# Optimization experiments

Measured on AMD Instinct MI355X. Metric: run time of the kernel, lower is better.

Reference implementation:

```python
import jax, jax.numpy as jnp
import numpy as np

B, T, C, H = 128, 256, 1024, 64


def setup_inputs() -> dict:
    key = jax.random.key(0)
    k1, k2, k3, k4 = jax.random.split(key, 4)
    # Glorot-ish scale for weights
    s = 1.0 / np.sqrt(C)
    return {
        "x": jax.random.normal(k1, (B, T, C), dtype=jnp.float32),
        "Wk": jax.random.normal(k2, (C, H), dtype=jnp.float32) * s,
        "Wq": jax.random.normal(k3, (C, H), dtype=jnp.float32) * s,
        "Wv": jax.random.normal(k4, (C, H), dtype=jnp.float32) * s,
    }


def reference(x, Wk, Wq, Wv):
    # Projections (no bias, matching use_bias=False)
    k = jnp.einsum("btc,ch->bth", x, Wk)  # [B,T,H]
    q = jnp.einsum("btc,ch->bth", x, Wq)
    v = jnp.einsum("btc,ch->bth", x, Wv)
    scale = k.shape[-1] ** -0.5
    wei = jnp.einsum("bth,bsh->bts", q, k) * scale  # [B,T,T]
    t = x.shape[1]
    causal = jnp.tril(jnp.ones((t, t), dtype=bool))
    wei = jnp.where(causal, wei, -jnp.inf)
    wei = jax.nn.softmax(wei, axis=-1)
    # dropout is identity at inference
    out = jnp.einsum("bts,bsh->bth", wei, v)  # [B,T,H]
    return out
```

## Files before the change

kernel.cpp:

```cpp
#include <hip/hip_runtime.h>
#include <hip/hip_bf16.h>

typedef __bf16 v8bf __attribute__((ext_vector_type(8)));
typedef float f32x16 __attribute__((ext_vector_type(16)));
typedef unsigned int uint;
typedef unsigned short ushort;

#define GLOAD16(gsrc, ldst)                                                       \
  __builtin_amdgcn_global_load_lds(                                               \
      (const __attribute__((address_space(1))) unsigned int*)(gsrc),              \
      (__attribute__((address_space(3))) unsigned int*)(ldst), 16, 0, 0)

__device__ inline f32x16 zero16() {
  f32x16 z;
#pragma unroll
  for (int i = 0; i < 16; i++) z[i] = 0.f;
  return z;
}

__device__ inline uint pack_bf16(float a, float b) {
  union { __bf16 h[2]; uint u; } c;
  c.h[0] = (__bf16)a;
  c.h[1] = (__bf16)b;
  return c.u;
}

__global__ void prep_wt(const float* __restrict__ Wq, const float* __restrict__ Wk,
                        const float* __restrict__ Wv, char* __restrict__ Wt_s) {
  __shared__ __bf16 tile[64][74];
  const int mat = blockIdx.x >> 4;
  const int c0 = (blockIdx.x & 15) * 64;
  const float* src = (mat == 0) ? Wq : (mat == 1) ? Wk : Wv;
  const int t = threadIdx.x;
  {
    const int r = t >> 2;
    const int ch = (t & 3) * 16;
    const float4* s4 = (const float4*)(src + (size_t)(c0 + r) * 64 + ch);
#pragma unroll
    for (int j = 0; j < 4; j++) {
      float4 f = s4[j];
      tile[r][ch + 4 * j + 0] = (__bf16)f.x;
      tile[r][ch + 4 * j + 1] = (__bf16)f.y;
      tile[r][ch + 4 * j + 2] = (__bf16)f.z;
      tile[r][ch + 4 * j + 3] = (__bf16)f.w;
    }
  }
  __syncthreads();
  const int h = t >> 2;
  const int cc = (t & 3) * 16;
  union { __bf16 o[16]; uint4 u[2]; } pk;
#pragma unroll
  for (int j = 0; j < 16; j++) pk.o[j] = tile[cc + j][h];
  const int n = mat * 64 + h;
  char* base = Wt_s + (size_t)n * 2048 + (c0 >> 6) * 128;
  const int bc = cc * 2;
  *(uint4*)(base + ((bc) ^ ((n & 7) << 4))) = pk.u[0];
  *(uint4*)(base + ((bc + 16) ^ ((n & 7) << 4))) = pk.u[1];
}

__launch_bounds__(256, 2)
__global__ void proj_kernel(const float* __restrict__ x, const char* __restrict__ Wt_s,
                            __bf16* __restrict__ KQV) {
  __shared__ char lds[65536];
  char* A0 = lds;
  char* A1 = lds + 8192;
  char* W0 = lds + 16384;
  char* W1 = lds + 40960;

  const int tid = threadIdx.x;
  const int lane = tid & 63;
  const int wave = tid >> 6;
  const int wm = wave >> 1;
  const int wn = wave & 1;
  const int row0 = blockIdx.x * 64;

  const int sr = tid >> 2;
  const int sc = tid & 3;
  const float4* xp = (const float4*)(x + (size_t)(row0 + sr) * 1024 + sc * 16);

  f32x16 acc[3];
#pragma unroll
  for (int i = 0; i < 3; i++) acc[i] = zero16();

  float4 rA[4], rB[4];

#define LOADA(rr, t)                                                              \
  {                                                                               \
    _Pragma("unroll") for (int j = 0; j < 4; j++) rr[j] = xp[(t) * 16 + j];       \
  }

#define GW(t, Wbuf)                                                               \
  {                                                                               \
    _Pragma("unroll") for (int j = 0; j < 6; j++) {                               \
      int idx = wave * 64 + j * 256 + lane;                                       \
      GLOAD16(Wt_s + (size_t)(idx >> 3) * 2048 + (t) * 128 + (idx & 7) * 16,      \
              Wbuf + wave * 1024 + j * 4096);                                     \
    }                                                                             \
  }

#define CVTWRITE(rr, Abuf)                                                        \
  {                                                                               \
    union { __bf16 h[16]; uint4 u[2]; } cv;                                       \
    _Pragma("unroll") for (int j = 0; j < 4; j++) {                               \
      cv.h[4 * j + 0] = (__bf16)rr[j].x;                                          \
      cv.h[4 * j + 1] = (__bf16)rr[j].y;                                          \
      cv.h[4 * j + 2] = (__bf16)rr[j].z;                                          \
      cv.h[4 * j + 3] = (__bf16)rr[j].w;                                          \
    }                                                                             \
    *(uint4*)(Abuf + sr * 128 + ((sc * 32) ^ ((sr & 7) << 4))) = cv.u[0];         \
    *(uint4*)(Abuf + sr * 128 + ((sc * 32 + 16) ^ ((sr & 7) << 4))) = cv.u[1];    \
  }

#define MMA(Abuf, Wbuf)                                                           \
  {                                                                               \
    _Pragma("unroll") for (int ks = 0; ks < 4; ks++) {                            \
      int arow = wm * 32 + (lane & 31);                                           \
      int kb = ks * 32 + ((lane >> 5) << 4);                                      \
      v8bf av = *(const v8bf*)(Abuf + arow * 128 + (kb ^ ((arow & 7) << 4)));     \
      _Pragma("unroll") for (int nf = 0; nf < 3; nf++) {                          \
        int brow = wn * 96 + nf * 32 + (lane & 31);                               \
        v8bf bv = *(const v8bf*)(Wbuf + brow * 128 + (kb ^ ((brow & 7) << 4)));   \
        acc[nf] = __builtin_amdgcn_mfma_f32_32x32x16_bf16(av, bv, acc[nf], 0, 0, 0); \
      }                                                                           \
    }                                                                             \
  }

  GW(0, W0);
  LOADA(rA, 0);
  CVTWRITE(rA, A0);
  __syncthreads();

  for (int t = 0; t < 16; t += 2) {
    GW(t + 1, W1);
    LOADA(rB, t + 1);
    __builtin_amdgcn_sched_barrier(0);
    MMA(A0, W0);
    CVTWRITE(rB, A1);
    __syncthreads();
    if (t + 2 < 16) {
      GW(t + 2, W0);
      LOADA(rA, t + 2);
    }
    __builtin_amdgcn_sched_barrier(0);
    MMA(A1, W1);
    if (t + 2 < 16) {
      CVTWRITE(rA, A0);
      __syncthreads();
    }
  }

#pragma unroll
  for (int nf = 0; nf < 3; nf++) {
#pragma unroll
    for (int r = 0; r < 16; r++) {
      int row = row0 + wm * 32 + (r & 3) + ((r >> 2) << 3) + ((lane >> 5) << 2);
      int col = wn * 96 + nf * 32 + (lane & 31);
      KQV[(size_t)row * 192 + col] = (__bf16)acc[nf][r];
    }
  }
#undef LOADA
#undef GW
#undef CVTWRITE
#undef MMA
}

__launch_bounds__(256, 1)
__global__ void attn_kernel(const __bf16* __restrict__ KQV, float* __restrict__ out) {
  __shared__ uint4 lds4[81920 / 16];
  char* Klds = (char*)lds4;
  char* Vlds = (char*)lds4 + 32768;
  char* Qlds = (char*)lds4 + 65536;

  const int tid = threadIdx.x;
  const int lane = tid & 63;
  const int wave = tid >> 6;
  const int b = blockIdx.x >> 1;
  const int half = blockIdx.x & 1;
  const int bt0 = half * 128;
  const size_t base = (size_t)b * 256 * 192;

  {
    int s = tid;
    const uint4* src = (const uint4*)(KQV + base + (size_t)s * 192 + 64);
#pragma unroll
    for (int i = 0; i < 8; i++) {
      uint4 v = src[i];
      int byte = s * 128 + ((i * 16) ^ ((s & 7) << 4));
      *(uint4*)(Klds + byte) = v;
    }
  }
  {
    int s = tid;
    const uint4* src = (const uint4*)(KQV + base + (size_t)s * 192 + 128);
#pragma unroll
    for (int i = 0; i < 8; i++) {
      uint4 v = src[i];
      const ushort* e = (const ushort*)&v;
#pragma unroll
      for (int j = 0; j < 8; j++) {
        int h = i * 8 + j;
        int byte = h * 512 + ((s * 2) ^ ((h & 7) << 4));
        *(ushort*)(Vlds + byte) = e[j];
      }
    }
  }
#pragma unroll
  for (int i = 0; i < 4; i++) {
    int c = tid + i * 256;
    int r = c >> 3, cc = c & 7;
    uint4 v = *(const uint4*)(KQV + base + (size_t)(bt0 + r) * 192 + cc * 8);
    int byte = r * 128 + ((cc * 16) ^ ((r & 7) << 4));
    *(uint4*)(Qlds + byte) = v;
  }
  __syncthreads();

  const int t0 = bt0 + wave * 32;
  const int tg = t0 + (lane & 31);
  const int nf = (t0 >> 5) + 1;

  f32x16 sacc[8];
#pragma unroll
  for (int sf = 0; sf < 8; sf++) {
    f32x16 sv = zero16();
    if (sf < nf) {
#pragma unroll
      for (int ks = 0; ks < 4; ks++) {
        int kbyte = ks * 32 + ((lane >> 5) << 4);
        int krow = sf * 32 + (lane & 31);
        v8bf a = *(const v8bf*)(Klds + krow * 128 + (kbyte ^ ((krow & 7) << 4)));
        int qrow = wave * 32 + (lane & 31);
        v8bf bq = *(const v8bf*)(Qlds + qrow * 128 + (kbyte ^ ((qrow & 7) << 4)));
        sv = __builtin_amdgcn_mfma_f32_32x32x16_bf16(a, bq, sv, 0, 0, 0);
      }
    }
    sacc[sf] = sv;
  }

  float m = -1e30f;
#pragma unroll
  for (int sf = 0; sf < 8; sf++) {
    if (sf < nf) {
#pragma unroll
      for (int r = 0; r < 16; r++) {
        int sg = sf * 32 + (r & 3) + ((r >> 2) << 3) + ((lane >> 5) << 2);
        float v = sacc[sf][r] * 0.125f;
        v = (sg > tg) ? -1e30f : v;
        sacc[sf][r] = v;
        m = fmaxf(m, v);
      }
    }
  }
  m = fmaxf(m, __shfl_xor(m, 32, 64));
  float l = 0.f;
#pragma unroll
  for (int sf = 0; sf < 8; sf++) {
    if (sf < nf) {
#pragma unroll
      for (int r = 0; r < 16; r++) {
        float p = __expf(sacc[sf][r] - m);
        sacc[sf][r] = p;
        l += p;
      }
    }
  }
  l += __shfl_xor(l, 32, 64);
  float inv = 1.0f / l;

  f32x16 oacc[2];
  oacc[0] = zero16();
  oacc[1] = zero16();
  const bool hiLane = (lane >= 32);
#pragma unroll
  for (int sf = 0; sf < 8; sf++) {
    if (sf < nf) {
      uint w[8], ow[8];
#pragma unroll
      for (int q = 0; q < 4; q++) {
        w[2 * q]     = pack_bf16(sacc[sf][4 * q] * inv,     sacc[sf][4 * q + 1] * inv);
        w[2 * q + 1] = pack_bf16(sacc[sf][4 * q + 2] * inv, sacc[sf][4 * q + 3] * inv);
      }
#pragma unroll
      for (int i = 0; i < 8; i++) ow[i] = (uint)__shfl_xor((int)w[i], 32, 64);
#pragma unroll
      for (int ks = 0; ks < 2; ks++) {
        int bse = 4 * ks;
        union { uint u[4]; v8bf v; } A;
        A.u[0] = hiLane ? ow[bse + 2] : w[bse + 0];
        A.u[1] = hiLane ? ow[bse + 3] : w[bse + 1];
        A.u[2] = hiLane ? w[bse + 2] : ow[bse + 0];
        A.u[3] = hiLane ? w[bse + 3] : ow[bse + 1];
        int sbyte0 = (sf * 32 + ks * 16) * 2 + ((lane >> 5) << 4);
#pragma unroll
        for (int hf = 0; hf < 2; hf++) {
          int vrow = hf * 32 + (lane & 31);
          v8bf bv = *(const v8bf*)(Vlds + vrow * 512 + (sbyte0 ^ ((vrow & 7) << 4)));
          oacc[hf] = __builtin_amdgcn_mfma_f32_32x32x16_bf16(A.v, bv, oacc[hf], 0, 0, 0);
        }
      }
    }
  }

#pragma unroll
  for (int hf = 0; hf < 2; hf++) {
#pragma unroll
    for (int r = 0; r < 16; r++) {
      int t = t0 + (r & 3) + ((r >> 2) << 3) + ((lane >> 5) << 2);
      int h = hf * 32 + (lane & 31);
      out[((size_t)b * 256 + t) * 64 + h] = oacc[hf][r];
    }
  }
}

extern "C" void kernel_launch(void* const* d_in, const int* in_sizes, int n_in,
                              void* d_out, int out_size, void* d_ws, size_t ws_size,
                              hipStream_t stream) {
  const float* x  = (const float*)d_in[0];
  const float* Wk = (const float*)d_in[1];
  const float* Wq = (const float*)d_in[2];
  const float* Wv = (const float*)d_in[3];
  float* out = (float*)d_out;

  __bf16* KQV = (__bf16*)d_ws;
  char* Wt_s  = (char*)d_ws + (size_t)32768 * 192 * 2;

  prep_wt<<<48, 256, 0, stream>>>(Wq, Wk, Wv, Wt_s);
  proj_kernel<<<512, 256, 0, stream>>>(x, Wt_s, KQV);
  attn_kernel<<<256, 256, 0, stream>>>(KQV, out);
}
```

Baseline: 46.74 us.

## Shrink projection tiles to 32 rows and restructure pipeline with explicit waitcnt barriers

```diff
diff --git a/kernel.cpp b/kernel.cpp
--- a/kernel.cpp
+++ b/kernel.cpp
@@ -58,21 +58,19 @@
   *(uint4*)(base + ((bc + 16) ^ ((n & 7) << 4))) = pk.u[1];
 }
 
-__launch_bounds__(256, 2)
+__launch_bounds__(128, 2)
 __global__ void proj_kernel(const float* __restrict__ x, const char* __restrict__ Wt_s,
                             __bf16* __restrict__ KQV) {
-  __shared__ char lds[65536];
+  __shared__ char lds[32768];
   char* A0 = lds;
-  char* A1 = lds + 8192;
-  char* W0 = lds + 16384;
-  char* W1 = lds + 40960;
+  char* A1 = lds + 4096;
+  char* Wb = lds + 8192;
 
   const int tid = threadIdx.x;
   const int lane = tid & 63;
   const int wave = tid >> 6;
-  const int wm = wave >> 1;
-  const int wn = wave & 1;
-  const int row0 = blockIdx.x * 64;
+  const int wn = wave;
+  const int row0 = blockIdx.x * 32;
 
   const int sr = tid >> 2;
   const int sc = tid & 3;
@@ -82,19 +80,21 @@
 #pragma unroll
   for (int i = 0; i < 3; i++) acc[i] = zero16();
 
-  float4 rA[4], rB[4];
-
-#define LOADA(rr, t)                                                              \
+  float4 sA[4], sB[4];
+
+#define SB_ __builtin_amdgcn_sched_barrier(0)
+
+#define LOADA(rr, T)                                                              \
   {                                                                               \
-    _Pragma("unroll") for (int j = 0; j < 4; j++) rr[j] = xp[(t) * 16 + j];       \
-  }
-
-#define GW(t, Wbuf)                                                               \
+    _Pragma("unroll") for (int j = 0; j < 4; j++) rr[j] = xp[(T) * 16 + j];       \
+  }
+
+#define GW(T)                                                                     \
   {                                                                               \
-    _Pragma("unroll") for (int j = 0; j < 6; j++) {                               \
-      int idx = wave * 64 + j * 256 + lane;                                       \
-      GLOAD16(Wt_s + (size_t)(idx >> 3) * 2048 + (t) * 128 + (idx & 7) * 16,      \
-              Wbuf + wave * 1024 + j * 4096);                                     \
+    _Pragma("unroll") for (int j = 0; j < 12; j++) {                              \
+      int idx = j * 128 + wave * 64 + lane;                                       \
+      GLOAD16(Wt_s + (size_t)(idx >> 3) * 2048 + (T) * 128 + (idx & 7) * 16,      \
+              Wb + j * 2048 + wave * 1024);                                       \
     }                                                                             \
   }
 
@@ -111,57 +111,95 @@
     *(uint4*)(Abuf + sr * 128 + ((sc * 32 + 16) ^ ((sr & 7) << 4))) = cv.u[1];    \
   }
 
-#define MMA(Abuf, Wbuf)                                                           \
+#define MMA(Abuf)                                                                 \
   {                                                                               \
     _Pragma("unroll") for (int ks = 0; ks < 4; ks++) {                            \
-      int arow = wm * 32 + (lane & 31);                                           \
+      int arow = lane & 31;                                                       \
       int kb = ks * 32 + ((lane >> 5) << 4);                                      \
       v8bf av = *(const v8bf*)(Abuf + arow * 128 + (kb ^ ((arow & 7) << 4)));     \
       _Pragma("unroll") for (int nf = 0; nf < 3; nf++) {                          \
         int brow = wn * 96 + nf * 32 + (lane & 31);                               \
-        v8bf bv = *(const v8bf*)(Wbuf + brow * 128 + (kb ^ ((brow & 7) << 4)));   \
+        v8bf bv = *(const v8bf*)(Wb + brow * 128 + (kb ^ ((brow & 7) << 4)));     \
         acc[nf] = __builtin_amdgcn_mfma_f32_32x32x16_bf16(av, bv, acc[nf], 0, 0, 0); \
       }                                                                           \
     }                                                                             \
   }
 
-  GW(0, W0);
-  LOADA(rA, 0);
-  CVTWRITE(rA, A0);
-  __syncthreads();
-
-  for (int t = 0; t < 16; t += 2) {
-    GW(t + 1, W1);
-    LOADA(rB, t + 1);
-    __builtin_amdgcn_sched_barrier(0);
-    MMA(A0, W0);
-    CVTWRITE(rB, A1);
-    __syncthreads();
-    if (t + 2 < 16) {
-      GW(t + 2, W0);
-      LOADA(rA, t + 2);
-    }
-    __builtin_amdgcn_sched_barrier(0);
-    MMA(A1, W1);
-    if (t + 2 < 16) {
-      CVTWRITE(rA, A0);
-      __syncthreads();
-    }
-  }
+#define BAR_A                                                                     \
+  do {                                                                            \
+    asm volatile("s_waitcnt lgkmcnt(0)" ::: "memory");                            \
+    __builtin_amdgcn_s_barrier();                                                 \
+    SB_;                                                                          \
+  } while (0)
+#define BARW4                                                                     \
+  do {                                                                            \
+    asm volatile("s_waitcnt vmcnt(4) lgkmcnt(0)" ::: "memory");                   \
+    __builtin_amdgcn_s_barrier();                                                 \
+    SB_;                                                                          \
+  } while (0)
+#define BARW0                                                                     \
+  do {                                                                            \
+    asm volatile("s_waitcnt vmcnt(0) lgkmcnt(0)" ::: "memory");                   \
+    __builtin_amdgcn_s_barrier();                                                 \
+    SB_;                                                                          \
+  } while (0)
+
+#define STEP(T, ACUR, ANXT, SCONS, SFILL)                                         \
+  MMA(ACUR);                                                                      \
+  CVTWRITE(SCONS, ANXT);                                                          \
+  BAR_A;                                                                          \
+  GW(T + 1);                                                                      \
+  SB_;                                                                            \
+  LOADA(SFILL, T + 2);                                                            \
+  BARW4;
+
+  GW(0);
+  SB_;
+  LOADA(sA, 0);
+  LOADA(sB, 1);
+  SB_;
+  CVTWRITE(sA, A0);
+  BARW4;
+
+  STEP(0, A0, A1, sB, sA)
+  STEP(1, A1, A0, sA, sB)
+  STEP(2, A0, A1, sB, sA)
+  STEP(3, A1, A0, sA, sB)
+  STEP(4, A0, A1, sB, sA)
+  STEP(5, A1, A0, sA, sB)
+  STEP(6, A0, A1, sB, sA)
+  STEP(7, A1, A0, sA, sB)
+  STEP(8, A0, A1, sB, sA)
+  STEP(9, A1, A0, sA, sB)
+  STEP(10, A0, A1, sB, sA)
+  STEP(11, A1, A0, sA, sB)
+  STEP(12, A0, A1, sB, sA)
+  STEP(13, A1, A0, sA, sB)
+  MMA(A0);
+  CVTWRITE(sB, A1);
+  BAR_A;
+  GW(15);
+  BARW0;
+  MMA(A1);
 
 #pragma unroll
   for (int nf = 0; nf < 3; nf++) {
 #pragma unroll
     for (int r = 0; r < 16; r++) {
-      int row = row0 + wm * 32 + (r & 3) + ((r >> 2) << 3) + ((lane >> 5) << 2);
+      int row = row0 + (r & 3) + ((r >> 2) << 3) + ((lane >> 5) << 2);
       int col = wn * 96 + nf * 32 + (lane & 31);
       KQV[(size_t)row * 192 + col] = (__bf16)acc[nf][r];
     }
   }
+#undef STEP
+#undef BAR_A
+#undef BARW4
+#undef BARW0
 #undef LOADA
 #undef GW
 #undef CVTWRITE
 #undef MMA
+#undef SB_
 }
 
 __launch_bounds__(256, 1)
@@ -324,6 +362,6 @@
   char* Wt_s  = (char*)d_ws + (size_t)32768 * 192 * 2;
 
   prep_wt<<<48, 256, 0, stream>>>(Wq, Wk, Wv, Wt_s);
-  proj_kernel<<<512, 256, 0, stream>>>(x, Wt_s, KQV);
+  proj_kernel<<<1024, 128, 0, stream>>>(x, Wt_s, KQV);
   attn_kernel<<<256, 256, 0, stream>>>(KQV, out);
 }
```

Result: slower. 51.46 us, median of 2 (+10.1%).
